# Kernel optimization log

Hardware: AMD Instinct MI355X
Metric: run time of the kernel (lower is better)

The kernel has to match this reference:

```python
import jax, jax.numpy as jnp
import numpy as np

N_NODES = 50000
N_EDGES = 800000
IN_CH = 128
HID = 32
HEADS = 8
EMB = 64
NEG_SLOPE = 0.2


def _segment_softmax(e, seg, num_segments):
    # e: [E, H] edge scores, seg: [E] destination node ids
    m = jax.ops.segment_max(e, seg, num_segments=num_segments)
    ex = jnp.exp(e - m[seg])
    denom = jax.ops.segment_sum(ex, seg, num_segments=num_segments)
    return ex / (denom[seg] + 1e-16)


def gat_conv(x, src, dst, W, a_src, a_dst, bias, heads, out_ch):
    # x: [N, F_in]; W: [F_in, heads*out_ch]; a_src/a_dst: [heads, out_ch]; bias: [heads*out_ch]
    n = x.shape[0]
    h = (x @ W).reshape(n, heads, out_ch)                 # [N, H, C]
    alpha_src = jnp.sum(h * a_src[None], axis=-1)         # [N, H]
    alpha_dst = jnp.sum(h * a_dst[None], axis=-1)         # [N, H]
    e = jax.nn.leaky_relu(alpha_src[src] + alpha_dst[dst], NEG_SLOPE)  # [E, H]
    alpha = _segment_softmax(e, dst, n)                   # [E, H]
    msg = h[src] * alpha[:, :, None]                      # [E, H, C]
    out = jax.ops.segment_sum(msg, dst, num_segments=n)   # [N, H, C]
    return out.reshape(n, heads * out_ch) + bias


def _with_self_loops(edge_index, n):
    # PyG GATConv default add_self_loops=True
    loop = jnp.arange(n, dtype=edge_index.dtype)
    src = jnp.concatenate([edge_index[0], loop])
    dst = jnp.concatenate([edge_index[1], loop])
    return src, dst


def setup_inputs() -> dict:
    key = jax.random.key(0)
    ks = jax.random.split(key, 16)
    x = jax.random.normal(ks[0], (N_NODES, IN_CH), dtype=jnp.float32)
    edge_index = jax.random.randint(ks[1], (2, N_EDGES), 0, N_NODES, dtype=jnp.int32)

    def glorot(k, shape):
        fan = sum(shape[-2:]) if len(shape) >= 2 else shape[-1]
        return jax.random.normal(k, shape, dtype=jnp.float32) * jnp.sqrt(2.0 / fan)

    # conv1: IN_CH -> HID x HEADS (concat)
    W1 = glorot(ks[2], (IN_CH, HEADS * HID))
    a_src1 = glorot(ks[3], (HEADS, HID))
    a_dst1 = glorot(ks[4], (HEADS, HID))
    b1 = jnp.zeros((HEADS * HID,), jnp.float32)
    # conv2: HID*HEADS -> HID, heads=1
    W2 = glorot(ks[5], (HEADS * HID, HID))
    a_src2 = glorot(ks[6], (1, HID))
    a_dst2 = glorot(ks[7], (1, HID))
    b2 = jnp.zeros((HID,), jnp.float32)
    # conv3: HID -> EMB, heads=1
    W3 = glorot(ks[8], (HID, EMB))
    a_src3 = glorot(ks[9], (1, EMB))
    a_dst3 = glorot(ks[10], (1, EMB))
    b3 = jnp.zeros((EMB,), jnp.float32)
    return {"x": x, "edge_index": edge_index,
            "W1": W1, "a_src1": a_src1, "a_dst1": a_dst1, "b1": b1,
            "W2": W2, "a_src2": a_src2, "a_dst2": a_dst2, "b2": b2,
            "W3": W3, "a_src3": a_src3, "a_dst3": a_dst3, "b3": b3}


def reference(x, edge_index, W1, a_src1, a_dst1, b1, W2, a_src2, a_dst2, b2,
              W3, a_src3, a_dst3, b3):
    src, dst = _with_self_loops(edge_index, x.shape[0])
    h = gat_conv(x, src, dst, W1, a_src1, a_dst1, b1, HEADS, HID)
    h = jax.nn.elu(h)  # dropout is identity in eval mode
    h = gat_conv(h, src, dst, W2, a_src2, a_dst2, b2, 1, HID)
    h = jax.nn.elu(h)
    out = gat_conv(h, src, dst, W3, a_src3, a_dst3, b3, 1, EMB)
    return out
```

## Files before the change

### kernel.cpp

```cpp
#include <hip/hip_runtime.h>
#include <hip/hip_bf16.h>
#include <math.h>

#define N_NODES 50000
#define N_EDGES 800000
#define ET (N_EDGES + N_NODES)
#define F0 128
#define H1 8
#define C1 32
#define D1 (H1*C1)
#define C2 32
#define C3 64
#define CAP 128
#define GEMMB 391
#define SCATB 1661

typedef unsigned short u16;
typedef unsigned int u32;
typedef __attribute__((ext_vector_type(8))) short short8;
typedef __attribute__((ext_vector_type(4))) float f32x4;

__device__ __forceinline__ float lrelu(float x) { return x >= 0.f ? x : 0.2f * x; }
__device__ __forceinline__ float eluf(float x)  { return x > 0.f ? x : (expf(x) - 1.f); }

__device__ __forceinline__ u16 f2bf(float f) {
    u32 u = __float_as_uint(f);
    return (u16)((u + 0x7FFFu + ((u >> 16) & 1u)) >> 16);
}
__device__ __forceinline__ u32 pack2bf(float lo, float hi) {
    return ((u32)f2bf(hi) << 16) | (u32)f2bf(lo);
}
__device__ __forceinline__ float bf2f(u16 v) {
    return __uint_as_float((u32)v << 16);
}
__device__ __forceinline__ float4 bf4_to_f4(uint2 v) {
    float4 r;
    r.x = __uint_as_float(v.x << 16);
    r.y = __uint_as_float(v.x & 0xFFFF0000u);
    r.z = __uint_as_float(v.y << 16);
    r.w = __uint_as_float(v.y & 0xFFFF0000u);
    return r;
}


__global__ void prep_kernel(const float* __restrict__ W1, const float* __restrict__ W2,
                            const float* __restrict__ W3,
                            u16* __restrict__ W1t, u16* __restrict__ W2t, u16* __restrict__ W3t,
                            int* __restrict__ cnt) {
    int t = blockIdx.x * 256 + threadIdx.x;
    if (t < N_NODES) cnt[t] = 0;
    if (t < F0 * D1) {
        int n = t >> 7, k = t & 127;
        W1t[n * F0 + k] = f2bf(W1[(size_t)k * D1 + n]);
    }
    if (t < D1 * C2) {
        int k = t >> 5, n = t & 31;
        W2t[n * D1 + k] = f2bf(W2[t]);
    }
    if (t < C2 * C3) {
        int k = t >> 6, n = t & 63;
        W3t[n * C2 + k] = f2bf(W3[t]);
    }
}


#define WKS 136

__global__ __launch_bounds__(512, 2) void gemm1_scat(const u16* __restrict__ W1t,
                                                     const float* __restrict__ x,
                                                     const float* __restrict__ aS1,
                                                     const float* __restrict__ aD1,
                                                     u16* __restrict__ h1b,
                                                     float* __restrict__ as,
                                                     float* __restrict__ ad, int M,
                                                     const int* __restrict__ srcArr,
                                                     const int* __restrict__ dstArr,
                                                     int* __restrict__ cnt,
                                                     int* __restrict__ csrF) {
    __shared__ u16 Wt[128][WKS];
    int tid = threadIdx.x;

    if (blockIdx.x >= GEMMB) {
        int e = (blockIdx.x - GEMMB) * 512 + tid;
        if (e < ET) {
            int s, d;
            if (e < N_EDGES) { s = srcArr[e]; d = dstArr[e]; } else { s = d = e - N_EDGES; }
            int pos = atomicAdd(&cnt[d], 1);
            csrF[d * CAP + pos] = s;
        }
        return;
    }

    int bm = blockIdx.x * 128;

    int w = tid >> 6, lane = tid & 63, l15 = lane & 15, q = lane >> 4;
    int mr = bm + w * 16 + l15;
    if (mr > M - 1) mr = M - 1;

    short8 af[4];
#pragma unroll
    for (int kc = 0; kc < 4; ++kc) {
        const float* ap = x + (size_t)mr * F0 + kc * 32 + q * 8;
        float4 a0 = *(const float4*)ap;
        float4 a1 = *(const float4*)(ap + 4);
        af[kc][0] = (short)f2bf(a0.x); af[kc][1] = (short)f2bf(a0.y);
        af[kc][2] = (short)f2bf(a0.z); af[kc][3] = (short)f2bf(a0.w);
        af[kc][4] = (short)f2bf(a1.x); af[kc][5] = (short)f2bf(a1.y);
        af[kc][6] = (short)f2bf(a1.z); af[kc][7] = (short)f2bf(a1.w);
    }

    f32x4 acc[16];
#pragma unroll
    for (int t = 0; t < 16; ++t) acc[t] = (f32x4){0.f, 0.f, 0.f, 0.f};

#pragma unroll
    for (int half = 0; half < 2; ++half) {
        __syncthreads();
        for (int idx = tid; idx < 128 * F0 / 8; idx += 512) {
            int n = idx >> 4, c = idx & 15;
            *(short8*)&Wt[n][c * 8] =
                *(const short8*)(W1t + (size_t)(half * 128 + n) * F0 + c * 8);
        }
        __syncthreads();
#pragma unroll
        for (int t = 0; t < 8; ++t) {
#pragma unroll
            for (int kc = 0; kc < 4; ++kc) {
                short8 bf = *(const short8*)&Wt[t * 16 + l15][kc * 32 + q * 8];
                acc[half * 8 + t] =
                    __builtin_amdgcn_mfma_f32_16x16x32_bf16(af[kc], bf, acc[half * 8 + t], 0, 0, 0);
            }
        }
    }

#pragma unroll
    for (int r = 0; r < 4; ++r) {
        int row = bm + w * 16 + q * 4 + r;
        if (row >= M) continue;
        size_t base = (size_t)row * D1;
#pragma unroll
        for (int t = 0; t < 16; ++t)
            h1b[base + t * 16 + l15] = f2bf(acc[t][r]);
    }

#pragma unroll
    for (int lh = 0; lh < 8; ++lh) {
        float aS0  = aS1[lh * 32 + l15];
        float aS16 = aS1[lh * 32 + 16 + l15];
        float aD0  = aD1[lh * 32 + l15];
        float aD16 = aD1[lh * 32 + 16 + l15];
#pragma unroll
        for (int r = 0; r < 4; ++r) {
            float s1 = acc[2 * lh][r] * aS0 + acc[2 * lh + 1][r] * aS16;
            float s2 = acc[2 * lh][r] * aD0 + acc[2 * lh + 1][r] * aD16;
            s1 += __shfl_xor(s1, 1); s1 += __shfl_xor(s1, 2);
            s1 += __shfl_xor(s1, 4); s1 += __shfl_xor(s1, 8);
            s2 += __shfl_xor(s2, 1); s2 += __shfl_xor(s2, 2);
            s2 += __shfl_xor(s2, 4); s2 += __shfl_xor(s2, 8);
            int row = bm + w * 16 + q * 4 + r;
            if (l15 == 0 && row < M) {
                as[row * 8 + lh] = s1;
                ad[row * 8 + lh] = s2;
            }
        }
    }
}


__global__ __launch_bounds__(256) void gemm2_mfma(const u16* __restrict__ A,
                                                  const u16* __restrict__ W2t,
                                                  const float* __restrict__ aS2,
                                                  const float* __restrict__ aD2,
                                                  u16* __restrict__ h2b,
                                                  float* __restrict__ as,
                                                  float* __restrict__ ad, int M) {
    int tid = threadIdx.x;
    int bm = blockIdx.x * 64;
    int w = tid >> 6, lane = tid & 63, l15 = lane & 15, q = lane >> 4;
    int mr = bm + w * 16 + l15;
    if (mr > M - 1) mr = M - 1;

    f32x4 acc0 = {0.f, 0.f, 0.f, 0.f};
    f32x4 acc1 = {0.f, 0.f, 0.f, 0.f};
    const u16* b0p = W2t + (size_t)(0 * 16 + l15) * D1;
    const u16* b1p = W2t + (size_t)(1 * 16 + l15) * D1;
#pragma unroll
    for (int k0 = 0; k0 < D1; k0 += 32) {
        short8 af = *(const short8*)(A + (size_t)mr * D1 + k0 + q * 8);
        short8 b0 = *(const short8*)(b0p + k0 + q * 8);
        short8 b1 = *(const short8*)(b1p + k0 + q * 8);
        acc0 = __builtin_amdgcn_mfma_f32_16x16x32_bf16(af, b0, acc0, 0, 0, 0);
        acc1 = __builtin_amdgcn_mfma_f32_16x16x32_bf16(af, b1, acc1, 0, 0, 0);
    }

    float aS0 = aS2[l15], aS16 = aS2[16 + l15];
    float aD0 = aD2[l15], aD16 = aD2[16 + l15];
#pragma unroll
    for (int r = 0; r < 4; ++r) {
        int row = bm + w * 16 + q * 4 + r;
        float s1 = acc0[r] * aS0 + acc1[r] * aS16;
        float s2 = acc0[r] * aD0 + acc1[r] * aD16;
        s1 += __shfl_xor(s1, 1); s1 += __shfl_xor(s1, 2);
        s1 += __shfl_xor(s1, 4); s1 += __shfl_xor(s1, 8);
        s2 += __shfl_xor(s2, 1); s2 += __shfl_xor(s2, 2);
        s2 += __shfl_xor(s2, 4); s2 += __shfl_xor(s2, 8);
        if (row < M) {
            h2b[(size_t)row * C2 + 0 * 16 + l15] = f2bf(acc0[r]);
            h2b[(size_t)row * C2 + 1 * 16 + l15] = f2bf(acc1[r]);
            if (l15 == 0) { as[row] = s1; ad[row] = s2; }
        }
    }
}


__global__ __launch_bounds__(256) void agg1_kernel(const int* __restrict__ cnt, const int* __restrict__ csrF,
                                                   const u16* __restrict__ h, const float* __restrict__ as,
                                                   const float* __restrict__ ad, const float* __restrict__ bias,
                                                   u16* __restrict__ outb) {
    int node = blockIdx.x * 4 + (threadIdx.x >> 6);
    if (node >= N_NODES) return;
    int lane = threadIdx.x & 63;
    int hh = lane >> 3;
    int j  = lane & 7;
    int s0 = node * CAP;
    int deg = cnt[node];
    int dmain = deg < 64 ? deg : 64;
    int idxv = (lane < dmain) ? csrF[s0 + lane] : 0;
    float adw = ad[node * H1 + j];
    const u16* hb = h + hh * C1 + j * 4;

    int sAll[8];
#pragma unroll
    for (int r = 0; r < 8; ++r) sAll[r] = __shfl(idxv, r * 8 + hh);
    float aAll[8];
#pragma unroll
    for (int r = 0; r < 8; ++r) aAll[r] = as[sAll[r] * H1 + j];
    float wAll[8];
#pragma unroll
    for (int r = 0; r < 8; ++r)
        wAll[r] = (r * 8 + hh < dmain) ? __expf(lrelu(aAll[r] + adw)) : 0.f;

    float ws = wAll[0] + wAll[1] + wAll[2] + wAll[3]
             + wAll[4] + wAll[5] + wAll[6] + wAll[7];
    ws += __shfl_xor(ws, 8);
    ws += __shfl_xor(ws, 16);
    ws += __shfl_xor(ws, 32);
    float dsum = __shfl(ws, hh);

    float4 acc = make_float4(0.f, 0.f, 0.f, 0.f);
    for (int base = 0; base < dmain; base += 8) {
        int r = base >> 3;
        int su[8];
#pragma unroll
        for (int u = 0; u < 8; ++u) su[u] = __shfl(idxv, base + u);
        uint2 v[8];
#pragma unroll
        for (int u = 0; u < 8; ++u) v[u] = *(const uint2*)(hb + (size_t)su[u] * D1);
        float wr = wAll[0];
#pragma unroll
        for (int t = 1; t < 8; ++t) if (t == r) wr = wAll[t];
#pragma unroll
        for (int u = 0; u < 8; ++u) {
            float wv = __shfl(wr, u * 8 + hh);
            float4 hv = bf4_to_f4(v[u]);
            acc.x += wv * hv.x; acc.y += wv * hv.y;
            acc.z += wv * hv.z; acc.w += wv * hv.w;
        }
    }

    for (int i = 64; i < deg; ++i) {
        int s = csrF[s0 + i];
        float4 hv = bf4_to_f4(*(const uint2*)(hb + (size_t)s * D1));
        float w = __expf(lrelu(as[s * H1 + hh] + ad[node * H1 + hh]));
        dsum += w;
        acc.x += w * hv.x; acc.y += w * hv.y; acc.z += w * hv.z; acc.w += w * hv.w;
    }

    float inv = 1.f / (dsum + 1e-16f);
    int ob = node * D1 + hh * C1 + j * 4;
    const float* bp = bias + hh * C1 + j * 4;
    float rx = eluf(acc.x * inv + bp[0]);
    float ry = eluf(acc.y * inv + bp[1]);
    float rz = eluf(acc.z * inv + bp[2]);
    float rw = eluf(acc.w * inv + bp[3]);
    uint2 pr;
    pr.x = pack2bf(rx, ry);
    pr.y = pack2bf(rz, rw);
    *(uint2*)(outb + ob) = pr;
}


__global__ __launch_bounds__(256) void agg32_kernel(const int* __restrict__ cnt, const int* __restrict__ csrF,
                                                    const u16* __restrict__ h, const float* __restrict__ as,
                                                    const float* __restrict__ ad, const float* __restrict__ bias,
                                                    const u16* __restrict__ W3t,
                                                    const float* __restrict__ aS3,
                                                    const float* __restrict__ aD3,
                                                    u16* __restrict__ h3b,
                                                    float* __restrict__ as3,
                                                    float* __restrict__ ad3) {
    int node = blockIdx.x * 4 + (threadIdx.x >> 6);
    if (node >= N_NODES) return;
    int lane = threadIdx.x & 63;
    int eg = lane >> 3;
    int cg = lane & 7;
    int s0 = node * CAP;
    int deg = cnt[node];
    int dmain = deg < 64 ? deg : 64;
    int idxv = (lane < dmain) ? csrF[s0 + lane] : 0;
    float adv = ad[node];

    float4 acc = make_float4(0.f, 0.f, 0.f, 0.f);
    float dsum = 0.f;
    for (int base = 0; base < dmain; base += 16) {
        int i0 = base + eg;
        int i1 = base + eg + 8;
        int sa = __shfl(idxv, i0);
        int sb = __shfl(idxv, i1);
        uint2 va = *(const uint2*)(h + (size_t)sa * C2 + cg * 4);
        uint2 vb = *(const uint2*)(h + (size_t)sb * C2 + cg * 4);
        float wa = (i0 < dmain) ? __expf(lrelu(as[sa] + adv)) : 0.f;
        float wb = (i1 < dmain) ? __expf(lrelu(as[sb] + adv)) : 0.f;
        float4 ha = bf4_to_f4(va);
        float4 hb = bf4_to_f4(vb);
        dsum += wa + wb;
        acc.x += wa * ha.x + wb * hb.x;
        acc.y += wa * ha.y + wb * hb.y;
        acc.z += wa * ha.z + wb * hb.z;
        acc.w += wa * ha.w + wb * hb.w;
    }
    for (int i = 64 + eg; i < deg; i += 8) {
        int s = csrF[s0 + i];
        float4 hv = bf4_to_f4(*(const uint2*)(h + (size_t)s * C2 + cg * 4));
        float w = __expf(lrelu(as[s] + adv));
        dsum += w;
        acc.x += w * hv.x; acc.y += w * hv.y; acc.z += w * hv.z; acc.w += w * hv.w;
    }
#pragma unroll
    for (int o = 8; o < 64; o <<= 1) {
        acc.x += __shfl_xor(acc.x, o);
        acc.y += __shfl_xor(acc.y, o);
        acc.z += __shfl_xor(acc.z, o);
        acc.w += __shfl_xor(acc.w, o);
        dsum  += __shfl_xor(dsum, o);
    }

    float inv = 1.f / (dsum + 1e-16f);
    const float* bp = bias + cg * 4;
    float x30 = eluf(acc.x * inv + bp[0]);
    float x31 = eluf(acc.y * inv + bp[1]);
    float x32 = eluf(acc.z * inv + bp[2]);
    float x33 = eluf(acc.w * inv + bp[3]);

    short8 wv[4];
#pragma unroll
    for (int t = 0; t < 4; ++t) wv[t] = *(const short8*)(W3t + lane * C2 + t * 8);
    float o = 0.f;
#pragma unroll
    for (int qq = 0; qq < 8; ++qq) {
        float v0 = __shfl(x30, qq);
        float v1 = __shfl(x31, qq);
        float v2 = __shfl(x32, qq);
        float v3 = __shfl(x33, qq);
        o += v0 * bf2f((u16)wv[(qq * 4 + 0) >> 3][(qq * 4 + 0) & 7]);
        o += v1 * bf2f((u16)wv[(qq * 4 + 1) >> 3][(qq * 4 + 1) & 7]);
        o += v2 * bf2f((u16)wv[(qq * 4 + 2) >> 3][(qq * 4 + 2) & 7]);
        o += v3 * bf2f((u16)wv[(qq * 4 + 3) >> 3][(qq * 4 + 3) & 7]);
    }

    h3b[(size_t)node * C3 + lane] = f2bf(o);
    float s1 = o * aS3[lane];
    float s2 = o * aD3[lane];
#pragma unroll
    for (int of = 1; of < 64; of <<= 1) {
        s1 += __shfl_xor(s1, of);
        s2 += __shfl_xor(s2, of);
    }
    if (lane == 0) { as3[node] = s1; ad3[node] = s2; }
}


__global__ __launch_bounds__(256) void agg64_kernel(const int* __restrict__ cnt, const int* __restrict__ csrF,
                                                    const u16* __restrict__ h, const float* __restrict__ as,
                                                    const float* __restrict__ ad, const float* __restrict__ bias,
                                                    float* __restrict__ out) {
    int node = blockIdx.x * 4 + (threadIdx.x >> 6);
    if (node >= N_NODES) return;
    int lane = threadIdx.x & 63;
    int eg = lane >> 4;
    int cg = lane & 15;
    int s0 = node * CAP;
    int deg = cnt[node];
    int dmain = deg < 64 ? deg : 64;
    int idxv = (lane < dmain) ? csrF[s0 + lane] : 0;
    float adv = ad[node];

    float4 acc = make_float4(0.f, 0.f, 0.f, 0.f);
    float dsum = 0.f;
    for (int base = 0; base < dmain; base += 8) {
        int i0 = base + eg;
        int i1 = base + eg + 4;
        int sa = __shfl(idxv, i0);
        int sb = __shfl(idxv, i1);
        uint2 va = *(const uint2*)(h + (size_t)sa * C3 + cg * 4);
        uint2 vb = *(const uint2*)(h + (size_t)sb * C3 + cg * 4);
        float wa = (i0 < dmain) ? __expf(lrelu(as[sa] + adv)) : 0.f;
        float wb = (i1 < dmain) ? __expf(lrelu(as[sb] + adv)) : 0.f;
        float4 ha = bf4_to_f4(va);
        float4 hb = bf4_to_f4(vb);
        dsum += wa + wb;
        acc.x += wa * ha.x + wb * hb.x;
        acc.y += wa * ha.y + wb * hb.y;
        acc.z += wa * ha.z + wb * hb.z;
        acc.w += wa * ha.w + wb * hb.w;
    }
    for (int i = 64 + eg; i < deg; i += 4) {
        int s = csrF[s0 + i];
        float4 hv = bf4_to_f4(*(const uint2*)(h + (size_t)s * C3 + cg * 4));
        float w = __expf(lrelu(as[s] + adv));
        dsum += w;
        acc.x += w * hv.x; acc.y += w * hv.y; acc.z += w * hv.z; acc.w += w * hv.w;
    }
#pragma unroll
    for (int o = 16; o < 64; o <<= 1) {
        acc.x += __shfl_xor(acc.x, o);
        acc.y += __shfl_xor(acc.y, o);
        acc.z += __shfl_xor(acc.z, o);
        acc.w += __shfl_xor(acc.w, o);
        dsum  += __shfl_xor(dsum, o);
    }
    if (eg == 0) {
        float inv = 1.f / (dsum + 1e-16f);
        const float* bp = bias + cg * 4;
        float4 r;
        r.x = acc.x * inv + bp[0];
        r.y = acc.y * inv + bp[1];
        r.z = acc.z * inv + bp[2];
        r.w = acc.w * inv + bp[3];
        *(float4*)(out + (size_t)node * C3 + cg * 4) = r;
    }
}


extern "C" void kernel_launch(void* const* d_in, const int* in_sizes, int n_in,
                              void* d_out, int out_size, void* d_ws, size_t ws_size,
                              hipStream_t stream) {
    const float* x   = (const float*)d_in[0];
    const int*   ei  = (const int*)d_in[1];
    const float* W1  = (const float*)d_in[2];
    const float* aS1 = (const float*)d_in[3];
    const float* aD1 = (const float*)d_in[4];
    const float* b1  = (const float*)d_in[5];
    const float* W2  = (const float*)d_in[6];
    const float* aS2 = (const float*)d_in[7];
    const float* aD2 = (const float*)d_in[8];
    const float* b2  = (const float*)d_in[9];
    const float* W3  = (const float*)d_in[10];
    const float* aS3 = (const float*)d_in[11];
    const float* aD3 = (const float*)d_in[12];
    const float* b3  = (const float*)d_in[13];
    float* out = (float*)d_out;

    char* p = (char*)d_ws;
    auto alloc = [&](size_t bytes) -> void* {
        void* r = (void*)p;
        p += (bytes + 255) & ~(size_t)255;
        return r;
    };
    u16*   h1b  = (u16*)alloc((size_t)N_NODES * D1 * 2);
    u16*   x2b  = (u16*)alloc((size_t)N_NODES * D1 * 2);
    u16*   h2b  = (u16*)alloc((size_t)N_NODES * C2 * 2);
    u16*   h3b  = (u16*)alloc((size_t)N_NODES * C3 * 2);
    int*   cnt  = (int*)alloc((size_t)N_NODES * 4);
    int*   csrF = (int*)alloc((size_t)N_NODES * CAP * 4);
    float* asb  = (float*)alloc((size_t)N_NODES * H1 * 4);
    float* adb  = (float*)alloc((size_t)N_NODES * H1 * 4);
    float* as3b = (float*)alloc((size_t)N_NODES * 4);
    float* ad3b = (float*)alloc((size_t)N_NODES * 4);
    u16*   W1t  = (u16*)alloc((size_t)F0 * D1 * 2);
    u16*   W2t  = (u16*)alloc((size_t)D1 * C2 * 2);
    u16*   W3t  = (u16*)alloc((size_t)C2 * C3 * 2);

    const int* srcArr = ei;
    const int* dstArr = ei + N_EDGES;

    prep_kernel<<<(N_NODES + 255) / 256, 256, 0, stream>>>(W1, W2, W3, W1t, W2t, W3t, cnt);

    int nb4 = (N_NODES + 3) / 4;
    int mb64 = (N_NODES + 63) / 64;

    gemm1_scat<<<GEMMB + SCATB, 512, 0, stream>>>(W1t, x, aS1, aD1, h1b, asb, adb, N_NODES,
                                                  srcArr, dstArr, cnt, csrF);
    agg1_kernel<<<nb4, 256, 0, stream>>>(cnt, csrF, h1b, asb, adb, b1, x2b);

    gemm2_mfma<<<mb64, 256, 0, stream>>>(x2b, W2t, aS2, aD2, h2b, asb, adb, N_NODES);
    agg32_kernel<<<nb4, 256, 0, stream>>>(cnt, csrF, h2b, asb, adb, b2,
                                          W3t, aS3, aD3, h3b, as3b, ad3b);

    agg64_kernel<<<nb4, 256, 0, stream>>>(cnt, csrF, h3b, as3b, ad3b, b3, out);
}
```

Before: 297.5 us.

## Fuse layer-2 GEMM into agg1 epilogue and fold weight prep into gemm1

```diff
diff --git a/kernel.cpp b/kernel.cpp
--- a/kernel.cpp
+++ b/kernel.cpp
@@ -43,31 +43,10 @@
 }
 
 
-__global__ void prep_kernel(const float* __restrict__ W1, const float* __restrict__ W2,
-                            const float* __restrict__ W3,
-                            u16* __restrict__ W1t, u16* __restrict__ W2t, u16* __restrict__ W3t,
-                            int* __restrict__ cnt) {
-    int t = blockIdx.x * 256 + threadIdx.x;
-    if (t < N_NODES) cnt[t] = 0;
-    if (t < F0 * D1) {
-        int n = t >> 7, k = t & 127;
-        W1t[n * F0 + k] = f2bf(W1[(size_t)k * D1 + n]);
-    }
-    if (t < D1 * C2) {
-        int k = t >> 5, n = t & 31;
-        W2t[n * D1 + k] = f2bf(W2[t]);
-    }
-    if (t < C2 * C3) {
-        int k = t >> 6, n = t & 63;
-        W3t[n * C2 + k] = f2bf(W3[t]);
-    }
-}
-
-
 #define WKS 136
 
-__global__ __launch_bounds__(512, 2) void gemm1_scat(const u16* __restrict__ W1t,
-                                                     const float* __restrict__ x,
+__global__ __launch_bounds__(512, 2) void gemm1_scat(const float* __restrict__ x,
+                                                     const float* __restrict__ W1,
                                                      const float* __restrict__ aS1,
                                                      const float* __restrict__ aD1,
                                                      u16* __restrict__ h1b,
@@ -76,12 +55,27 @@
                                                      const int* __restrict__ srcArr,
                                                      const int* __restrict__ dstArr,
                                                      int* __restrict__ cnt,
-                                                     int* __restrict__ csrF) {
+                                                     int* __restrict__ csrF,
+                                                     const float* __restrict__ W2,
+                                                     const float* __restrict__ W3,
+                                                     u16* __restrict__ W2t,
+                                                     u16* __restrict__ W3t) {
     __shared__ u16 Wt[128][WKS];
     int tid = threadIdx.x;
 
-    if (blockIdx.x >= GEMMB) {
-        int e = (blockIdx.x - GEMMB) * 512 + tid;
+    if (blockIdx.x == GEMMB) {
+        for (int idx = tid; idx < D1 * C2; idx += 512) {
+            int k = idx >> 5, n = idx & 31;
+            W2t[n * D1 + k] = f2bf(W2[idx]);
+        }
+        for (int idx = tid; idx < C2 * C3; idx += 512) {
+            int k = idx >> 6, n = idx & 63;
+            W3t[n * C2 + k] = f2bf(W3[idx]);
+        }
+        return;
+    }
+    if (blockIdx.x > GEMMB) {
+        int e = (blockIdx.x - GEMMB - 1) * 512 + tid;
         if (e < ET) {
             int s, d;
             if (e < N_EDGES) { s = srcArr[e]; d = dstArr[e]; } else { s = d = e - N_EDGES; }
@@ -116,10 +110,9 @@
 #pragma unroll
     for (int half = 0; half < 2; ++half) {
         __syncthreads();
-        for (int idx = tid; idx < 128 * F0 / 8; idx += 512) {
-            int n = idx >> 4, c = idx & 15;
-            *(short8*)&Wt[n][c * 8] =
-                *(const short8*)(W1t + (size_t)(half * 128 + n) * F0 + c * 8);
+        for (int idx = tid; idx < 128 * F0; idx += 512) {
+            int n = idx & 127, k = idx >> 7;
+            Wt[n][k] = f2bf(W1[(size_t)k * D1 + half * 128 + n]);
         }
         __syncthreads();
 #pragma unroll
@@ -167,56 +160,15 @@
 }
 
 
-__global__ __launch_bounds__(256) void gemm2_mfma(const u16* __restrict__ A,
-                                                  const u16* __restrict__ W2t,
-                                                  const float* __restrict__ aS2,
-                                                  const float* __restrict__ aD2,
-                                                  u16* __restrict__ h2b,
-                                                  float* __restrict__ as,
-                                                  float* __restrict__ ad, int M) {
-    int tid = threadIdx.x;
-    int bm = blockIdx.x * 64;
-    int w = tid >> 6, lane = tid & 63, l15 = lane & 15, q = lane >> 4;
-    int mr = bm + w * 16 + l15;
-    if (mr > M - 1) mr = M - 1;
-
-    f32x4 acc0 = {0.f, 0.f, 0.f, 0.f};
-    f32x4 acc1 = {0.f, 0.f, 0.f, 0.f};
-    const u16* b0p = W2t + (size_t)(0 * 16 + l15) * D1;
-    const u16* b1p = W2t + (size_t)(1 * 16 + l15) * D1;
-#pragma unroll
-    for (int k0 = 0; k0 < D1; k0 += 32) {
-        short8 af = *(const short8*)(A + (size_t)mr * D1 + k0 + q * 8);
-        short8 b0 = *(const short8*)(b0p + k0 + q * 8);
-        short8 b1 = *(const short8*)(b1p + k0 + q * 8);
-        acc0 = __builtin_amdgcn_mfma_f32_16x16x32_bf16(af, b0, acc0, 0, 0, 0);
-        acc1 = __builtin_amdgcn_mfma_f32_16x16x32_bf16(af, b1, acc1, 0, 0, 0);
-    }
-
-    float aS0 = aS2[l15], aS16 = aS2[16 + l15];
-    float aD0 = aD2[l15], aD16 = aD2[16 + l15];
-#pragma unroll
-    for (int r = 0; r < 4; ++r) {
-        int row = bm + w * 16 + q * 4 + r;
-        float s1 = acc0[r] * aS0 + acc1[r] * aS16;
-        float s2 = acc0[r] * aD0 + acc1[r] * aD16;
-        s1 += __shfl_xor(s1, 1); s1 += __shfl_xor(s1, 2);
-        s1 += __shfl_xor(s1, 4); s1 += __shfl_xor(s1, 8);
-        s2 += __shfl_xor(s2, 1); s2 += __shfl_xor(s2, 2);
-        s2 += __shfl_xor(s2, 4); s2 += __shfl_xor(s2, 8);
-        if (row < M) {
-            h2b[(size_t)row * C2 + 0 * 16 + l15] = f2bf(acc0[r]);
-            h2b[(size_t)row * C2 + 1 * 16 + l15] = f2bf(acc1[r]);
-            if (l15 == 0) { as[row] = s1; ad[row] = s2; }
-        }
-    }
-}
-
-
 __global__ __launch_bounds__(256) void agg1_kernel(const int* __restrict__ cnt, const int* __restrict__ csrF,
                                                    const u16* __restrict__ h, const float* __restrict__ as,
                                                    const float* __restrict__ ad, const float* __restrict__ bias,
-                                                   u16* __restrict__ outb) {
+                                                   const u16* __restrict__ W2t,
+                                                   const float* __restrict__ aS2,
+                                                   const float* __restrict__ aD2,
+                                                   u16* __restrict__ h2b,
+                                                   float* __restrict__ as2,
+                                                   float* __restrict__ ad2) {
     int node = blockIdx.x * 4 + (threadIdx.x >> 6);
     if (node >= N_NODES) return;
     int lane = threadIdx.x & 63;
@@ -277,16 +229,44 @@
     }
 
     float inv = 1.f / (dsum + 1e-16f);
-    int ob = node * D1 + hh * C1 + j * 4;
     const float* bp = bias + hh * C1 + j * 4;
     float rx = eluf(acc.x * inv + bp[0]);
     float ry = eluf(acc.y * inv + bp[1]);
     float rz = eluf(acc.z * inv + bp[2]);
     float rw = eluf(acc.w * inv + bp[3]);
-    uint2 pr;
-    pr.x = pack2bf(rx, ry);
-    pr.y = pack2bf(rz, rw);
-    *(uint2*)(outb + ob) = pr;
+
+    int c = lane & 31;
+    int hbase = lane & 32;
+    const u16* w2p = W2t + (size_t)c * D1 + (hbase ? 128 : 0);
+    float p = 0.f;
+#pragma unroll
+    for (int g = 0; g < 4; ++g) {
+        short8 wv2[4];
+#pragma unroll
+        for (int t = 0; t < 4; ++t) wv2[t] = *(const short8*)(w2p + g * 32 + t * 8);
+#pragma unroll
+        for (int s8 = 0; s8 < 8; ++s8) {
+            int src = hbase + g * 8 + s8;
+            float v0 = __shfl(rx, src);
+            float v1 = __shfl(ry, src);
+            float v2 = __shfl(rz, src);
+            float v3 = __shfl(rw, src);
+            const int db = s8 * 4;
+            p += v0 * bf2f((u16)wv2[db >> 3][db & 7]);
+            p += v1 * bf2f((u16)wv2[(db + 1) >> 3][(db + 1) & 7]);
+            p += v2 * bf2f((u16)wv2[(db + 2) >> 3][(db + 2) & 7]);
+            p += v3 * bf2f((u16)wv2[(db + 3) >> 3][(db + 3) & 7]);
+        }
+    }
+    p += __shfl_xor(p, 32);
+    if (lane < 32) h2b[(size_t)node * C2 + c] = f2bf(p);
+    float s1 = p * aS2[c];
+    float s2 = p * aD2[c];
+    s1 += __shfl_xor(s1, 1); s1 += __shfl_xor(s1, 2); s1 += __shfl_xor(s1, 4);
+    s1 += __shfl_xor(s1, 8); s1 += __shfl_xor(s1, 16);
+    s2 += __shfl_xor(s2, 1); s2 += __shfl_xor(s2, 2); s2 += __shfl_xor(s2, 4);
+    s2 += __shfl_xor(s2, 8); s2 += __shfl_xor(s2, 16);
+    if (lane == 0) { as2[node] = s1; ad2[node] = s2; }
 }
 
 
@@ -468,34 +448,32 @@
         return r;
     };
     u16*   h1b  = (u16*)alloc((size_t)N_NODES * D1 * 2);
-    u16*   x2b  = (u16*)alloc((size_t)N_NODES * D1 * 2);
     u16*   h2b  = (u16*)alloc((size_t)N_NODES * C2 * 2);
     u16*   h3b  = (u16*)alloc((size_t)N_NODES * C3 * 2);
     int*   cnt  = (int*)alloc((size_t)N_NODES * 4);
     int*   csrF = (int*)alloc((size_t)N_NODES * CAP * 4);
     float* asb  = (float*)alloc((size_t)N_NODES * H1 * 4);
     float* adb  = (float*)alloc((size_t)N_NODES * H1 * 4);
+    float* as2b = (float*)alloc((size_t)N_NODES * 4);
+    float* ad2b = (float*)alloc((size_t)N_NODES * 4);
     float* as3b = (float*)alloc((size_t)N_NODES * 4);
     float* ad3b = (float*)alloc((size_t)N_NODES * 4);
-    u16*   W1t  = (u16*)alloc((size_t)F0 * D1 * 2);
     u16*   W2t  = (u16*)alloc((size_t)D1 * C2 * 2);
     u16*   W3t  = (u16*)alloc((size_t)C2 * C3 * 2);
 
     const int* srcArr = ei;
     const int* dstArr = ei + N_EDGES;
 
-    prep_kernel<<<(N_NODES + 255) / 256, 256, 0, stream>>>(W1, W2, W3, W1t, W2t, W3t, cnt);
-
     int nb4 = (N_NODES + 3) / 4;
-    int mb64 = (N_NODES + 63) / 64;
-
-    gemm1_scat<<<GEMMB + SCATB, 512, 0, stream>>>(W1t, x, aS1, aD1, h1b, asb, adb, N_NODES,
-                                                  srcArr, dstArr, cnt, csrF);
-    agg1_kernel<<<nb4, 256, 0, stream>>>(cnt, csrF, h1b, asb, adb, b1, x2b);
-
-    gemm2_mfma<<<mb64, 256, 0, stream>>>(x2b, W2t, aS2, aD2, h2b, asb, adb, N_NODES);
-    agg32_kernel<<<nb4, 256, 0, stream>>>(cnt, csrF, h2b, asb, adb, b2,
+
+    hipMemsetAsync(cnt, 0, (size_t)N_NODES * 4, stream);
+
+    gemm1_scat<<<GEMMB + 1 + SCATB, 512, 0, stream>>>(x, W1, aS1, aD1, h1b, asb, adb, N_NODES,
+                                                      srcArr, dstArr, cnt, csrF,
+                                                      W2, W3, W2t, W3t);
+    agg1_kernel<<<nb4, 256, 0, stream>>>(cnt, csrF, h1b, asb, adb, b1,
+                                         W2t, aS2, aD2, h2b, as2b, ad2b);
+    agg32_kernel<<<nb4, 256, 0, stream>>>(cnt, csrF, h2b, as2b, ad2b, b2,
                                           W3t, aS3, aD3, h3b, as3b, ad3b);
-
     agg64_kernel<<<nb4, 256, 0, stream>>>(cnt, csrF, h3b, as3b, ad3b, b3, out);
 }
```

Measured after the change: 339.5 us. +14.1%, slower.
